# Kernel optimization log

Hardware: AMD Instinct MI355X
Metric: run time of the kernel (lower is better)

## Reference

```python
import jax, jax.numpy as jnp
import numpy as np

N = 500_000      # total points
B = 64           # graphs in batch
D_IN = 64        # input feature dim (conv.in_tensor_reps.dim)
D_HID = 128      # EdgeConv MLP hidden
D_OUT = 128      # EdgeConv MLP out


def setup_inputs() -> dict:
    key = jax.random.key(0)
    k = jax.random.split(key, 8)
    x = jax.random.normal(k[0], (N, D_IN), jnp.float32)
    pos = jax.random.normal(k[1], (N, 3), jnp.float32)
    batch = jnp.sort(jax.random.randint(k[2], (N,), 0, B, dtype=jnp.int32))
    lframes = jax.random.normal(k[3], (N, 3, 3), jnp.float32)
    fan1 = 2 * D_IN + 3
    W1 = jax.random.normal(k[4], (fan1, D_HID), jnp.float32) / np.sqrt(fan1)
    b1 = jnp.zeros((D_HID,), jnp.float32)
    W2 = jax.random.normal(k[5], (D_HID, D_OUT), jnp.float32) / np.sqrt(D_HID)
    b2 = jnp.zeros((D_OUT,), jnp.float32)
    return {"x": x, "pos": pos, "batch": batch, "lframes": lframes,
            "W1": W1, "b1": b1, "W2": W2, "b2": b2}


def reference(x, pos, batch, lframes, W1, b1, W2, b2):
    n = pos.shape[0]
    # scatter-mean: center of mass per graph
    counts = jax.ops.segment_sum(jnp.ones((n,), pos.dtype), batch, num_segments=B)
    coms = jax.ops.segment_sum(pos, batch, num_segments=B) / jnp.maximum(counts, 1.0)[:, None]
    # distance of each point to its graph's COM
    dist = jnp.linalg.norm(pos - coms[batch], axis=-1)
    # scatter-min argmin per graph (first occurrence, like torch_scatter.scatter_min)
    min_d = jax.ops.segment_min(dist, batch, num_segments=B)
    node_ids = jnp.arange(n, dtype=jnp.int32)
    cand = jnp.where(dist <= min_d[batch], node_ids, n)
    idx = jnp.minimum(jax.ops.segment_min(cand, batch, num_segments=B), n - 1)  # [B]
    # gathers for the destination (center) nodes
    x_dst = x[idx]          # [B, D_IN]
    pos_dst = pos[idx]      # [B, 3]
    lframes_dst = lframes[idx]  # [B, 3, 3]
    # EdgeConv over edge_index = [arange(N) -> batch]:
    # message_e = MLP([x_dst_i, x_src_j - x_dst_i, pos_j - pos_i]), max-aggregated per graph
    xd = x_dst[batch]                      # [N, D_IN]
    feat = jnp.concatenate([xd, x - xd, pos - pos_dst[batch]], axis=-1)  # [N, 2*D_IN+3]
    h = jax.nn.relu(feat @ W1 + b1)        # [N, D_HID]
    msg = h @ W2 + b2                      # [N, D_OUT]
    out = jax.ops.segment_max(msg, batch, num_segments=B)  # [B, D_OUT]
    return out, pos_dst, batch[idx], lframes_dst
```

## Files before the change

### kernel.cpp

```cpp
#include <hip/hip_runtime.h>
#include <hip/hip_bf16.h>

#define NPTS 500000
#define NGR  64
#define TR   256
#define NT2  ((NPTS + TR - 1) / TR)
#define GRID2 256

typedef __bf16 bf16x8 __attribute__((ext_vector_type(8)));
typedef float f32x4 __attribute__((ext_vector_type(4)));
typedef unsigned int u32x4 __attribute__((ext_vector_type(4)));

#define OFF_BOUNDS 0
#define OFF_OUTACC 6144
#define OFF_CBIAS  38912
#define OFF_W1PT   71680
#define OFF_W1AT   73728
#define OFF_W2T    90112

__device__ __forceinline__ unsigned mapf(float f) {
    union { float f; unsigned u; } v; v.f = f;
    return ((int)v.u >= 0) ? (v.u | 0x80000000u) : ~v.u;
}

#define GLOAD_LDS16(g, l) __builtin_amdgcn_global_load_lds(                 \
    (__attribute__((address_space(1))) void*)(g),                           \
    (__attribute__((address_space(3))) void*)(l), 16, 0, 0)

__global__ void k_prep(const float* __restrict__ W1,
                       const float* __restrict__ W2,
                       const int* __restrict__ batch,
                       unsigned short* __restrict__ W1aT,
                       unsigned short* __restrict__ W2T,
                       float* __restrict__ W1pT,
                       int* __restrict__ bounds,
                       unsigned* __restrict__ outacc) {
    int i = blockIdx.x * 256 + threadIdx.x;
    if (i < 8192) outacc[i] = 0u;
    if (blockIdx.x == 0 && threadIdx.x < 65) {
        int target = threadIdx.x;
        int lo = 0, hi = NPTS;
        while (lo < hi) {
            int mid = (lo + hi) >> 1;
            if (batch[mid] < target) lo = mid + 1; else hi = mid;
        }
        bounds[threadIdx.x] = lo;
    }
    if (i < 8192) {
        int n = i >> 6;
        unsigned short v = (unsigned short)(__builtin_bit_cast(unsigned, (float)(__bf16)W1[(64 + (i & 63)) * 128 + n]) >> 16);
        W1aT[i ^ ((n & 7) << 3)] = v;
    } else if (i < 8192 + 16384) {
        int j = i - 8192; int n = j >> 7, k = j & 127;
        unsigned short v = (unsigned short)(__builtin_bit_cast(unsigned, (float)(__bf16)W2[k * 128 + n]) >> 16);
        W2T[j ^ ((n & 7) << 3)] = v;
    } else if (i < 8192 + 16384 + 512) {
        int j = i - 24576; int n = j >> 2, q = j & 3;
        W1pT[j] = (q < 3) ? W1[(128 + q) * 128 + n] : 0.f;
    }
}

__global__ void k_pre(const float* __restrict__ pos,
                      const int* __restrict__ batch,
                      const float* __restrict__ x,
                      const float* __restrict__ W1,
                      const float* __restrict__ b1,
                      const float* __restrict__ lfr,
                      const int* __restrict__ bounds,
                      float* __restrict__ cbias,
                      float* __restrict__ outf) {
    __shared__ double sd[4][3];
    __shared__ unsigned long long sk[4];
    __shared__ double scom[3];
    __shared__ int sid;
    __shared__ float sposd[3];

    int g = blockIdx.x, t = threadIdx.x;
    int lane = t & 63, wv = t >> 6;
    int s = bounds[g], e = bounds[g + 1];

    double sx = 0.0, sy = 0.0, sz = 0.0;
    for (int i = s + t; i < e; i += 256) {
        sx += (double)pos[i * 3 + 0];
        sy += (double)pos[i * 3 + 1];
        sz += (double)pos[i * 3 + 2];
    }
    #pragma unroll
    for (int m = 1; m < 64; m <<= 1) {
        sx += __shfl_xor(sx, m);
        sy += __shfl_xor(sy, m);
        sz += __shfl_xor(sz, m);
    }
    if (lane == 0) { sd[wv][0] = sx; sd[wv][1] = sy; sd[wv][2] = sz; }
    __syncthreads();
    if (t == 0) {
        double cnt = (double)(e - s);
        double rc = 1.0 / (cnt > 1.0 ? cnt : 1.0);
        scom[0] = (sd[0][0] + sd[1][0] + sd[2][0] + sd[3][0]) * rc;
        scom[1] = (sd[0][1] + sd[1][1] + sd[2][1] + sd[3][1]) * rc;
        scom[2] = (sd[0][2] + sd[1][2] + sd[2][2] + sd[3][2]) * rc;
    }
    __syncthreads();
    double cx = scom[0], cy = scom[1], cz = scom[2];

    unsigned long long key = ~0ULL;
    for (int i = s + t; i < e; i += 256) {
        double dx = (double)pos[i * 3 + 0] - cx;
        double dy = (double)pos[i * 3 + 1] - cy;
        double dz = (double)pos[i * 3 + 2] - cz;
        double d2 = __builtin_fma(dx, dx, __builtin_fma(dy, dy, dz * dz));
        unsigned long long b = __builtin_bit_cast(unsigned long long, d2);
        unsigned long long k2 = (b & ~0xFFFFFULL) | (unsigned long long)i;
        key = k2 < key ? k2 : key;
    }
    #pragma unroll
    for (int m = 1; m < 64; m <<= 1) {
        unsigned long long o = __shfl_xor(key, m);
        key = o < key ? o : key;
    }
    if (lane == 0) sk[wv] = key;
    __syncthreads();
    if (t == 0) {
        unsigned long long k = sk[0];
        if (sk[1] < k) k = sk[1];
        if (sk[2] < k) k = sk[2];
        if (sk[3] < k) k = sk[3];
        int id = (int)(k & 0xFFFFFULL);
        if (id > NPTS - 1) id = NPTS - 1;
        sid = id;
    }
    __syncthreads();
    int id = sid;

    if (t < 3) {
        float p = pos[id * 3 + t];
        sposd[t] = p;
        outf[8192 + g * 3 + t] = p;
    }
    if (t == 4) outf[8192 + 192 + g] = (float)batch[id];
    if (t < 9) outf[8192 + 256 + g * 9 + t] = lfr[id * 9 + t];
    __syncthreads();

    if (t < 128) {
        int c = t;
        float sv = b1[c];
        for (int k = 0; k < 64; ++k) {
            float xd = x[id * 64 + k];
            sv += xd * (W1[k * 128 + c] - W1[(64 + k) * 128 + c]);
        }
        sv -= sposd[0] * W1[128 * 128 + c] + sposd[1] * W1[129 * 128 + c] + sposd[2] * W1[130 * 128 + c];
        cbias[g * 128 + c] = sv;
    }
}

__global__ __launch_bounds__(512, 2) void k_main(
    const float* __restrict__ x,
    const float* __restrict__ pos,
    const int* __restrict__ batch,
    const unsigned short* __restrict__ W1aT,
    const unsigned short* __restrict__ W2T,
    const float* __restrict__ W1pT,
    const float* __restrict__ cbias,
    unsigned* __restrict__ outacc)
{
    __shared__ alignas(16) unsigned char smem[118784];

    const int tid  = threadIdx.x;
    const int w    = tid >> 6;
    const int lane = tid & 63;
    const int quad = lane >> 4;
    const int mr   = lane & 15;

    #pragma unroll
    for (int i = 0; i < 2; ++i)
        GLOAD_LDS16((const char*)W1aT + (i * 512 + tid) * 16,
                    (char*)smem + (i * 512 + tid) * 16);
    #pragma unroll
    for (int i = 0; i < 4; ++i)
        GLOAD_LDS16((const char*)W2T + (i * 512 + tid) * 16,
                    (char*)smem + 16384 + (i * 512 + tid) * 16);

    bf16x8 bfrE[8];
    #pragma unroll
    for (int t8 = 0; t8 < 8; ++t8) {
        f32x4 wp = *(const f32x4*)(W1pT + (t8 * 16 + mr) * 4);
        bf16x8 e = (bf16x8){0, 0, 0, 0, 0, 0, 0, 0};
        if (quad == 0) { e[0] = (__bf16)wp[0]; e[1] = (__bf16)wp[1]; e[2] = (__bf16)wp[2]; }
        bfrE[t8] = e;
    }

    __syncthreads();

    const unsigned short* sW1 = (const unsigned short*)smem;
    const unsigned short* sW2 = (const unsigned short*)(smem + 16384);
    __bf16* hsb = (__bf16*)(smem + 49152) + w * 4352;

    for (int t = blockIdx.x; t < NT2; t += GRID2) {
        const int row0 = t * TR + 32 * w;

        f32x4 av[2][4];
        #pragma unroll
        for (int u = 0; u < 2; ++u) {
            int gr2 = row0 + 16 * u + mr; if (gr2 > NPTS - 1) gr2 = NPTS - 1;
            const float* xp = x + gr2 * 64 + quad * 8;
            av[u][0] = *(const f32x4*)(xp);
            av[u][1] = *(const f32x4*)(xp + 4);
            av[u][2] = *(const f32x4*)(xp + 32);
            av[u][3] = *(const f32x4*)(xp + 36);
        }

        int rowg[2][4]; bool rowv[2][4];
        #pragma unroll
        for (int u = 0; u < 2; ++u)
            #pragma unroll
            for (int r = 0; r < 4; ++r) {
                int gr = row0 + 16 * u + quad * 4 + r;
                rowv[u][r] = (gr < NPTS);
                rowg[u][r] = batch[gr < NPTS ? gr : NPTS - 1];
            }
        int gf = batch[row0 < NPTS ? row0 : NPTS - 1];
        int rl = row0 + 31; if (rl > NPTS - 1) rl = NPTS - 1;
        int gl = batch[rl];
        float cb0[8];
        #pragma unroll
        for (int t8 = 0; t8 < 8; ++t8) cb0[t8] = cbias[gf * 128 + t8 * 16 + mr];
        float pE[2][3];
        #pragma unroll
        for (int u = 0; u < 2; ++u) {
            int gp = row0 + 16 * u + mr; if (gp > NPTS - 1) gp = NPTS - 1;
            pE[u][0] = pos[gp * 3 + 0];
            pE[u][1] = pos[gp * 3 + 1];
            pE[u][2] = pos[gp * 3 + 2];
        }

        bf16x8 afr[2][2];
        #pragma unroll
        for (int u = 0; u < 2; ++u)
            #pragma unroll
            for (int h = 0; h < 2; ++h) {
                f32x4 va = av[u][2 * h], vb = av[u][2 * h + 1];
                bf16x8 a;
                a[0] = (__bf16)va[0]; a[1] = (__bf16)va[1]; a[2] = (__bf16)va[2]; a[3] = (__bf16)va[3];
                a[4] = (__bf16)vb[0]; a[5] = (__bf16)vb[1]; a[6] = (__bf16)vb[2]; a[7] = (__bf16)vb[3];
                afr[u][h] = a;
            }

        f32x4 acc[2][8];
        #pragma unroll
        for (int u = 0; u < 2; ++u)
            #pragma unroll
            for (int t8 = 0; t8 < 8; ++t8) acc[u][t8] = (f32x4){0.f, 0.f, 0.f, 0.f};
        #pragma unroll
        for (int t8 = 0; t8 < 8; ++t8) {
            int n = t8 * 16 + mr;
            int sw = (n & 7) << 3;
            bf16x8 bv0 = __builtin_bit_cast(bf16x8, *(const u32x4*)(sW1 + ((n * 64 + quad * 8) ^ sw)));
            bf16x8 bv1 = __builtin_bit_cast(bf16x8, *(const u32x4*)(sW1 + ((n * 64 + 32 + quad * 8) ^ sw)));
            #pragma unroll
            for (int u = 0; u < 2; ++u) {
                acc[u][t8] = __builtin_amdgcn_mfma_f32_16x16x32_bf16(afr[u][0], bv0, acc[u][t8], 0, 0, 0);
                acc[u][t8] = __builtin_amdgcn_mfma_f32_16x16x32_bf16(afr[u][1], bv1, acc[u][t8], 0, 0, 0);
            }
        }
        bf16x8 aE[2];
        #pragma unroll
        for (int u = 0; u < 2; ++u) {
            bf16x8 a = (bf16x8){0, 0, 0, 0, 0, 0, 0, 0};
            if (quad == 0) { a[0] = (__bf16)pE[u][0]; a[1] = (__bf16)pE[u][1]; a[2] = (__bf16)pE[u][2]; }
            aE[u] = a;
        }
        #pragma unroll
        for (int t8 = 0; t8 < 8; ++t8)
            #pragma unroll
            for (int u = 0; u < 2; ++u)
                acc[u][t8] = __builtin_amdgcn_mfma_f32_16x16x32_bf16(aE[u], bfrE[t8], acc[u][t8], 0, 0, 0);

        #pragma unroll
        for (int u = 0; u < 2; ++u)
            #pragma unroll
            for (int r = 0; r < 4; ++r) {
                int lrow = 16 * u + quad * 4 + r;
                int g = rowg[u][r];
                bool odd = (g != gf);
                #pragma unroll
                for (int t8 = 0; t8 < 8; ++t8) {
                    float cbv = cb0[t8];
                    if (odd) cbv = cbias[g * 128 + t8 * 16 + mr];
                    float v = fmaxf(acc[u][t8][r] + cbv, 0.f);
                    hsb[lrow * 136 + t8 * 16 + mr] = (__bf16)v;
                }
            }

        f32x4 acc2[2][8];
        #pragma unroll
        for (int u = 0; u < 2; ++u)
            #pragma unroll
            for (int t8 = 0; t8 < 8; ++t8) acc2[u][t8] = (f32x4){0.f, 0.f, 0.f, 0.f};
        const unsigned short* hss = (const unsigned short*)hsb;
        #pragma unroll
        for (int kk = 0; kk < 4; ++kk) {
            bf16x8 a2[2];
            #pragma unroll
            for (int u = 0; u < 2; ++u)
                a2[u] = __builtin_bit_cast(bf16x8, *(const u32x4*)(hss + (16 * u + mr) * 136 + kk * 32 + quad * 8));
            #pragma unroll
            for (int t8 = 0; t8 < 8; ++t8) {
                int n = t8 * 16 + mr;
                bf16x8 bv = __builtin_bit_cast(bf16x8, *(const u32x4*)(sW2 + ((n * 128 + kk * 32 + quad * 8) ^ ((n & 7) << 3))));
                #pragma unroll
                for (int u = 0; u < 2; ++u)
                    acc2[u][t8] = __builtin_amdgcn_mfma_f32_16x16x32_bf16(a2[u], bv, acc2[u][t8], 0, 0, 0);
            }
        }

        for (int g = gf; g <= gl; ++g) {
            #pragma unroll
            for (int t8 = 0; t8 < 8; ++t8) {
                float m = -INFINITY;
                #pragma unroll
                for (int u = 0; u < 2; ++u)
                    #pragma unroll
                    for (int r = 0; r < 4; ++r)
                        if (rowv[u][r] && rowg[u][r] == g) m = fmaxf(m, acc2[u][t8][r]);
                m = fmaxf(m, __shfl_xor(m, 16));
                m = fmaxf(m, __shfl_xor(m, 32));
                unsigned mb = __builtin_bit_cast(unsigned, m);
                if (quad == 0 && mb != 0xFF800000u)
                    atomicMax(&outacc[g * 128 + t8 * 16 + mr], mapf(m));
            }
        }
    }
}

__global__ void k_out(const unsigned* __restrict__ outacc,
                      const float* __restrict__ b2v,
                      float* __restrict__ outf) {
    int i = blockIdx.x * 256 + threadIdx.x;
    unsigned key = outacc[i];
    float v;
    if (key == 0u) {
        v = -300.f;
    } else {
        unsigned bits = (key & 0x80000000u) ? (key & 0x7FFFFFFFu) : ~key;
        union { unsigned u; float f; } c; c.u = bits; v = c.f;
    }
    outf[i] = v + b2v[i & 127];
}

extern "C" void kernel_launch(void* const* d_in, const int* in_sizes, int n_in,
                              void* d_out, int out_size, void* d_ws, size_t ws_size,
                              hipStream_t stream) {
    const float* x   = (const float*)d_in[0];
    const float* pos = (const float*)d_in[1];
    const int*   bat = (const int*)d_in[2];
    const float* lfr = (const float*)d_in[3];
    const float* W1  = (const float*)d_in[4];
    const float* b1  = (const float*)d_in[5];
    const float* W2  = (const float*)d_in[6];
    const float* b2v = (const float*)d_in[7];
    float* outf = (float*)d_out;

    char* ws = (char*)d_ws;
    int*            bounds = (int*)(ws + OFF_BOUNDS);
    unsigned*       outacc = (unsigned*)(ws + OFF_OUTACC);
    float*          cbias  = (float*)(ws + OFF_CBIAS);
    float*          W1pT   = (float*)(ws + OFF_W1PT);
    unsigned short* W1aT   = (unsigned short*)(ws + OFF_W1AT);
    unsigned short* W2T    = (unsigned short*)(ws + OFF_W2T);

    k_prep<<<98, 256, 0, stream>>>(W1, W2, bat, W1aT, W2T, W1pT, bounds, outacc);
    k_pre<<<64, 256, 0, stream>>>(pos, bat, x, W1, b1, lfr, bounds, cbias, outf);
    k_main<<<GRID2, 512, 0, stream>>>(x, pos, bat, W1aT, W2T, W1pT, cbias, outacc);
    k_out<<<32, 256, 0, stream>>>(outacc, b2v, outf);
}
```

Baseline: 278.6 us.

## Merge prep into pre kernel and fold output finalization into main

The weight-prep work and the per-graph boundary search move into the per-graph preprocessing kernel, which now runs with 1024 threads per block and computes its own segment bounds. The output conversion kernel is replaced by a last-block-done counter at the end of the main kernel, so the final block decodes the accumulated maxima and adds the bias. This cuts the launch count from four to two and widens the COM/argmin and bias reductions. In exchange it adds a global atomic counter plus fence, and a serial tail executed by a single block.

```diff
diff --git a/kernel.cpp b/kernel.cpp
--- a/kernel.cpp
+++ b/kernel.cpp
@@ -11,7 +11,7 @@
 typedef float f32x4 __attribute__((ext_vector_type(4)));
 typedef unsigned int u32x4 __attribute__((ext_vector_type(4)));
 
-#define OFF_BOUNDS 0
+#define OFF_DONE   4096
 #define OFF_OUTACC 6144
 #define OFF_CBIAS  38912
 #define OFF_W1PT   71680
@@ -27,60 +27,64 @@
     (__attribute__((address_space(1))) void*)(g),                           \
     (__attribute__((address_space(3))) void*)(l), 16, 0, 0)
 
-__global__ void k_prep(const float* __restrict__ W1,
-                       const float* __restrict__ W2,
-                       const int* __restrict__ batch,
-                       unsigned short* __restrict__ W1aT,
-                       unsigned short* __restrict__ W2T,
-                       float* __restrict__ W1pT,
-                       int* __restrict__ bounds,
-                       unsigned* __restrict__ outacc) {
-    int i = blockIdx.x * 256 + threadIdx.x;
-    if (i < 8192) outacc[i] = 0u;
-    if (blockIdx.x == 0 && threadIdx.x < 65) {
-        int target = threadIdx.x;
+__global__ __launch_bounds__(1024) void k_pre(
+                      const float* __restrict__ pos,
+                      const int* __restrict__ batch,
+                      const float* __restrict__ x,
+                      const float* __restrict__ W1,
+                      const float* __restrict__ b1,
+                      const float* __restrict__ W2,
+                      const float* __restrict__ lfr,
+                      unsigned short* __restrict__ W1aT,
+                      unsigned short* __restrict__ W2T,
+                      float* __restrict__ W1pT,
+                      unsigned* __restrict__ outacc,
+                      unsigned* __restrict__ done,
+                      float* __restrict__ cbias,
+                      float* __restrict__ outf) {
+    __shared__ double sd[16][3];
+    __shared__ unsigned long long sk[16];
+    __shared__ double scom[3];
+    __shared__ int sid;
+    __shared__ float sposd[3];
+    __shared__ float sp[4][128];
+    __shared__ int sse[2];
+
+    int g = blockIdx.x, t = threadIdx.x;
+    int lane = t & 63, wv = t >> 6;
+
+    {
+        int i = g * 1024 + t;
+        if (i == 0) *done = 0u;
+        if (i < 8192) {
+            outacc[i] = 0u;
+            int n = i >> 6, k = i & 63;
+            unsigned short v = (unsigned short)(__builtin_bit_cast(unsigned, (float)(__bf16)W1[(64 + k) * 128 + n]) >> 16);
+            W1aT[i ^ ((n & 7) << 3)] = v;
+        } else if (i < 8192 + 16384) {
+            int j = i - 8192; int n = j >> 7, k = j & 127;
+            unsigned short v = (unsigned short)(__builtin_bit_cast(unsigned, (float)(__bf16)W2[k * 128 + n]) >> 16);
+            W2T[j ^ ((n & 7) << 3)] = v;
+        } else if (i < 8192 + 16384 + 512) {
+            int j = i - 24576; int n = j >> 2, q = j & 3;
+            W1pT[j] = (q < 3) ? W1[(128 + q) * 128 + n] : 0.f;
+        }
+    }
+
+    if (t < 2) {
+        int target = g + t;
         int lo = 0, hi = NPTS;
         while (lo < hi) {
             int mid = (lo + hi) >> 1;
             if (batch[mid] < target) lo = mid + 1; else hi = mid;
         }
-        bounds[threadIdx.x] = lo;
-    }
-    if (i < 8192) {
-        int n = i >> 6;
-        unsigned short v = (unsigned short)(__builtin_bit_cast(unsigned, (float)(__bf16)W1[(64 + (i & 63)) * 128 + n]) >> 16);
-        W1aT[i ^ ((n & 7) << 3)] = v;
-    } else if (i < 8192 + 16384) {
-        int j = i - 8192; int n = j >> 7, k = j & 127;
-        unsigned short v = (unsigned short)(__builtin_bit_cast(unsigned, (float)(__bf16)W2[k * 128 + n]) >> 16);
-        W2T[j ^ ((n & 7) << 3)] = v;
-    } else if (i < 8192 + 16384 + 512) {
-        int j = i - 24576; int n = j >> 2, q = j & 3;
-        W1pT[j] = (q < 3) ? W1[(128 + q) * 128 + n] : 0.f;
-    }
-}
-
-__global__ void k_pre(const float* __restrict__ pos,
-                      const int* __restrict__ batch,
-                      const float* __restrict__ x,
-                      const float* __restrict__ W1,
-                      const float* __restrict__ b1,
-                      const float* __restrict__ lfr,
-                      const int* __restrict__ bounds,
-                      float* __restrict__ cbias,
-                      float* __restrict__ outf) {
-    __shared__ double sd[4][3];
-    __shared__ unsigned long long sk[4];
-    __shared__ double scom[3];
-    __shared__ int sid;
-    __shared__ float sposd[3];
-
-    int g = blockIdx.x, t = threadIdx.x;
-    int lane = t & 63, wv = t >> 6;
-    int s = bounds[g], e = bounds[g + 1];
+        sse[t] = lo;
+    }
+    __syncthreads();
+    int s = sse[0], e = sse[1];
 
     double sx = 0.0, sy = 0.0, sz = 0.0;
-    for (int i = s + t; i < e; i += 256) {
+    for (int i = s + t; i < e; i += 1024) {
         sx += (double)pos[i * 3 + 0];
         sy += (double)pos[i * 3 + 1];
         sz += (double)pos[i * 3 + 2];
@@ -94,17 +98,17 @@
     if (lane == 0) { sd[wv][0] = sx; sd[wv][1] = sy; sd[wv][2] = sz; }
     __syncthreads();
     if (t == 0) {
+        double ax = 0.0, ay = 0.0, az = 0.0;
+        for (int q = 0; q < 16; ++q) { ax += sd[q][0]; ay += sd[q][1]; az += sd[q][2]; }
         double cnt = (double)(e - s);
         double rc = 1.0 / (cnt > 1.0 ? cnt : 1.0);
-        scom[0] = (sd[0][0] + sd[1][0] + sd[2][0] + sd[3][0]) * rc;
-        scom[1] = (sd[0][1] + sd[1][1] + sd[2][1] + sd[3][1]) * rc;
-        scom[2] = (sd[0][2] + sd[1][2] + sd[2][2] + sd[3][2]) * rc;
+        scom[0] = ax * rc; scom[1] = ay * rc; scom[2] = az * rc;
     }
     __syncthreads();
     double cx = scom[0], cy = scom[1], cz = scom[2];
 
     unsigned long long key = ~0ULL;
-    for (int i = s + t; i < e; i += 256) {
+    for (int i = s + t; i < e; i += 1024) {
         double dx = (double)pos[i * 3 + 0] - cx;
         double dy = (double)pos[i * 3 + 1] - cy;
         double dz = (double)pos[i * 3 + 2] - cz;
@@ -122,9 +126,7 @@
     __syncthreads();
     if (t == 0) {
         unsigned long long k = sk[0];
-        if (sk[1] < k) k = sk[1];
-        if (sk[2] < k) k = sk[2];
-        if (sk[3] < k) k = sk[3];
+        for (int q = 1; q < 16; ++q) if (sk[q] < k) k = sk[q];
         int id = (int)(k & 0xFFFFFULL);
         if (id > NPTS - 1) id = NPTS - 1;
         sid = id;
@@ -139,15 +141,22 @@
     }
     if (t == 4) outf[8192 + 192 + g] = (float)batch[id];
     if (t < 9) outf[8192 + 256 + g * 9 + t] = lfr[id * 9 + t];
-    __syncthreads();
-
+
+    if (t < 512) {
+        int c = t & 127, p = t >> 7;
+        float part = 0.f;
+        #pragma unroll
+        for (int kq = 0; kq < 16; ++kq) {
+            int k = p * 16 + kq;
+            float xd = x[id * 64 + k];
+            part += xd * (W1[k * 128 + c] - W1[(64 + k) * 128 + c]);
+        }
+        sp[p][c] = part;
+    }
+    __syncthreads();
     if (t < 128) {
         int c = t;
-        float sv = b1[c];
-        for (int k = 0; k < 64; ++k) {
-            float xd = x[id * 64 + k];
-            sv += xd * (W1[k * 128 + c] - W1[(64 + k) * 128 + c]);
-        }
+        float sv = b1[c] + sp[0][c] + sp[1][c] + sp[2][c] + sp[3][c];
         sv -= sposd[0] * W1[128 * 128 + c] + sposd[1] * W1[129 * 128 + c] + sposd[2] * W1[130 * 128 + c];
         cbias[g * 128 + c] = sv;
     }
@@ -161,9 +170,13 @@
     const unsigned short* __restrict__ W2T,
     const float* __restrict__ W1pT,
     const float* __restrict__ cbias,
-    unsigned* __restrict__ outacc)
+    unsigned* __restrict__ outacc,
+    unsigned* __restrict__ done,
+    const float* __restrict__ b2v,
+    float* __restrict__ outf)
 {
     __shared__ alignas(16) unsigned char smem[118784];
+    __shared__ unsigned sflag;
 
     const int tid  = threadIdx.x;
     const int w    = tid >> 6;
@@ -194,6 +207,7 @@
     const unsigned short* sW1 = (const unsigned short*)smem;
     const unsigned short* sW2 = (const unsigned short*)(smem + 16384);
     __bf16* hsb = (__bf16*)(smem + 49152) + w * 4352;
+    const unsigned short* hss = (const unsigned short*)hsb;
 
     for (int t = blockIdx.x; t < NT2; t += GRID2) {
         const int row0 = t * TR + 32 * w;
@@ -202,7 +216,7 @@
         #pragma unroll
         for (int u = 0; u < 2; ++u) {
             int gr2 = row0 + 16 * u + mr; if (gr2 > NPTS - 1) gr2 = NPTS - 1;
-            const float* xp = x + gr2 * 64 + quad * 8;
+            const float* xp = x + (size_t)gr2 * 64 + quad * 8;
             av[u][0] = *(const f32x4*)(xp);
             av[u][1] = *(const f32x4*)(xp + 4);
             av[u][2] = *(const f32x4*)(xp + 32);
@@ -296,7 +310,6 @@
         for (int u = 0; u < 2; ++u)
             #pragma unroll
             for (int t8 = 0; t8 < 8; ++t8) acc2[u][t8] = (f32x4){0.f, 0.f, 0.f, 0.f};
-        const unsigned short* hss = (const unsigned short*)hsb;
         #pragma unroll
         for (int kk = 0; kk < 4; ++kk) {
             bf16x8 a2[2];
@@ -330,21 +343,24 @@
             }
         }
     }
-}
-
-__global__ void k_out(const unsigned* __restrict__ outacc,
-                      const float* __restrict__ b2v,
-                      float* __restrict__ outf) {
-    int i = blockIdx.x * 256 + threadIdx.x;
-    unsigned key = outacc[i];
-    float v;
-    if (key == 0u) {
-        v = -300.f;
-    } else {
-        unsigned bits = (key & 0x80000000u) ? (key & 0x7FFFFFFFu) : ~key;
-        union { unsigned u; float f; } c; c.u = bits; v = c.f;
-    }
-    outf[i] = v + b2v[i & 127];
+
+    __threadfence();
+    __syncthreads();
+    if (tid == 0) sflag = atomicAdd(done, 1u);
+    __syncthreads();
+    if (sflag == (unsigned)(gridDim.x - 1)) {
+        for (int i = tid; i < 8192; i += 512) {
+            unsigned key = atomicMax(&outacc[i], 0u);
+            float v;
+            if (key == 0u) {
+                v = -300.f;
+            } else {
+                unsigned bits = (key & 0x80000000u) ? (key & 0x7FFFFFFFu) : ~key;
+                union { unsigned u; float f; } c; c.u = bits; v = c.f;
+            }
+            outf[i] = v + b2v[i & 127];
+        }
+    }
 }
 
 extern "C" void kernel_launch(void* const* d_in, const int* in_sizes, int n_in,
@@ -361,15 +377,15 @@
     float* outf = (float*)d_out;
 
     char* ws = (char*)d_ws;
-    int*            bounds = (int*)(ws + OFF_BOUNDS);
+    unsigned*       done   = (unsigned*)(ws + OFF_DONE);
     unsigned*       outacc = (unsigned*)(ws + OFF_OUTACC);
     float*          cbias  = (float*)(ws + OFF_CBIAS);
     float*          W1pT   = (float*)(ws + OFF_W1PT);
     unsigned short* W1aT   = (unsigned short*)(ws + OFF_W1AT);
     unsigned short* W2T    = (unsigned short*)(ws + OFF_W2T);
 
-    k_prep<<<98, 256, 0, stream>>>(W1, W2, bat, W1aT, W2T, W1pT, bounds, outacc);
-    k_pre<<<64, 256, 0, stream>>>(pos, bat, x, W1, b1, lfr, bounds, cbias, outf);
-    k_main<<<GRID2, 512, 0, stream>>>(x, pos, bat, W1aT, W2T, W1pT, cbias, outacc);
-    k_out<<<32, 256, 0, stream>>>(outacc, b2v, outf);
+    k_pre<<<64, 1024, 0, stream>>>(pos, bat, x, W1, b1, W2, lfr,
+                                   W1aT, W2T, W1pT, outacc, done, cbias, outf);
+    k_main<<<GRID2, 512, 0, stream>>>(x, pos, bat, W1aT, W2T, W1pT, cbias,
+                                      outacc, done, b2v, outf);
 }
```

Result: slower. 320.8 us (+15.2%).
